# Kernel tuning notes

Hardware: AMD Instinct MI355X
Metric: run time of the kernel (lower is better)

The kernel has to match this reference:

```python
import jax, jax.numpy as jnp
import numpy as np

B, T, H, C = 2048, 1024, 512, 9
ZD, SD, GD = 128, 128, 16
COND = ZD + SD + GD  # hidden_fc input dim


def _gru_cell(x, h, w_ih, w_hh, b_ih, b_hh):
    # torch.nn.GRUCell math
    gi = x @ w_ih.T + b_ih          # [B, 3H]
    gh = h @ w_hh.T + b_hh          # [B, 3H]
    i_r, i_z, i_n = jnp.split(gi, 3, axis=-1)
    h_r, h_z, h_n = jnp.split(gh, 3, axis=-1)
    r = jax.nn.sigmoid(i_r + h_r)
    zg = jax.nn.sigmoid(i_z + h_z)
    n = jnp.tanh(i_n + r * h_n)
    return (1.0 - zg) * n + zg * h


def setup_inputs() -> dict:
    key = jax.random.key(0)
    ks = jax.random.split(key, 16)
    s = 0.05
    f32 = jnp.float32
    return {
        "z": jax.random.normal(ks[0], (B, ZD), f32),
        "skel_encoded": jax.random.normal(ks[1], (B, SD), f32),
        "skel": jax.random.uniform(ks[2], (B, T, C), f32),
        "cond": jax.random.normal(ks[3], (B, GD), f32),
        "rand_seq": jax.random.uniform(ks[4], (T, B, C), f32),
        "W_h": jax.random.normal(ks[5], (H, COND), f32) * s,
        "b_h": jnp.zeros((H,), f32),
        "w_ih1": jax.random.normal(ks[6], (3 * H, 2 * C), f32) * s,
        "w_hh1": jax.random.normal(ks[7], (3 * H, H), f32) * s,
        "b_ih1": jnp.zeros((3 * H,), f32),
        "b_hh1": jnp.zeros((3 * H,), f32),
        "w_ih2": jax.random.normal(ks[8], (3 * H, H), f32) * s,
        "w_hh2": jax.random.normal(ks[9], (3 * H, H), f32) * s,
        "b_ih2": jnp.zeros((3 * H,), f32),
        "b_hh2": jnp.zeros((3 * H,), f32),
        "W_out": jax.random.normal(ks[10], (C, H), f32) * s,
        "b_out": jnp.zeros((C,), f32),
    }


def reference(z, skel_encoded, skel, cond, rand_seq, W_h, b_h,
              w_ih1, w_hh1, b_ih1, b_hh1, w_ih2, w_hh2, b_ih2, b_hh2,
              W_out, b_out):
    b = z.shape[0]
    zc = jnp.concatenate([z.reshape(b, -1), skel_encoded, cond], axis=-1)
    h1_0 = jnp.tanh(zc @ W_h.T + b_h)                 # init hidden for gru1
    h2_0 = jnp.zeros_like(h1_0)                       # replaced at step 0
    out0 = jnp.zeros((b, C), z.dtype)
    skel_t = jnp.transpose(skel, (1, 0, 2))           # [T, B, C]

    def step(carry, xs):
        h1, h2, out = carry
        sk, rnd, i = xs
        x = jnp.concatenate([out, sk], axis=-1)       # [B, 2C]
        h1 = _gru_cell(x, h1, w_ih1, w_hh1, b_ih1, b_hh1)
        h2 = jnp.where(i == 0, h1, h2)                # hx[1] = hx[0] at i==0
        h2 = _gru_cell(h1, h2, w_ih2, w_hh2, b_ih2, b_hh2)
        note = jnp.tanh(h2) @ W_out.T + b_out         # out_fc (dropout=0 in eval)
        out = (jax.nn.sigmoid(note) - rnd > 0).astype(note.dtype)  # Bernoulli sample
        return (h1, h2, out), note

    _, notes = jax.lax.scan(step, (h1_0, h2_0, out0),
                            (skel_t, rand_seq, jnp.arange(T)))
    return jnp.transpose(notes, (1, 0, 2))            # [B, T, C]
```

## Files before the change

### kernel.cpp

```cpp
#include <hip/hip_runtime.h>
#include <math.h>

#define B_TOT 2048
#define T_LEN 1024
#define HID   512
#define CH    9
#define CONDK 272
#define K1X   (2*CH)
#define G3    1536
#define ROWS  8
#define NWG   (B_TOT/ROWS)
#define NTHR  512

#define SZ_W1T  ((HID + K1X) * G3)
#define SZ_W2T  ((2*HID) * G3)
#define SZ_WHT  (CONDK * HID)
#define OFF_W1T 0
#define OFF_W2T (OFF_W1T + SZ_W1T)
#define OFF_WHT (OFF_W2T + SZ_W2T)

__global__ void prep_kernel(const float* __restrict__ w_ih1, const float* __restrict__ w_hh1,
                            const float* __restrict__ w_ih2, const float* __restrict__ w_hh2,
                            const float* __restrict__ W_h, float* __restrict__ ws)
{
    int i = blockIdx.x * blockDim.x + threadIdx.x;
    const int total = SZ_W1T + SZ_W2T + SZ_WHT;
    if (i >= total) return;
    if (i < SZ_W1T) {
        int k = i / G3, g = i % G3;
        ws[OFF_W1T + i] = (k < HID) ? w_hh1[g*HID + k] : w_ih1[g*K1X + (k - HID)];
    } else if (i < SZ_W1T + SZ_W2T) {
        int j = i - SZ_W1T;
        int k = j / G3, g = j % G3;
        ws[OFF_W2T + j] = (k < HID) ? w_hh2[g*HID + k] : w_ih2[g*HID + (k - HID)];
    } else {
        int j = i - SZ_W1T - SZ_W2T;
        int k = j / HID, u = j % HID;
        ws[OFF_WHT + j] = W_h[u*CONDK + k];
    }
}

__device__ __forceinline__ float sigmf(float x) { return 1.0f / (1.0f + expf(-x)); }

__global__ __launch_bounds__(NTHR, 2)
void note_decoder_kernel(const float* __restrict__ z, const float* __restrict__ se,
                         const float* __restrict__ skel, const float* __restrict__ cond,
                         const float* __restrict__ rnd,
                         const float* __restrict__ b_h,
                         const float* __restrict__ b_ih1, const float* __restrict__ b_hh1,
                         const float* __restrict__ b_ih2, const float* __restrict__ b_hh2,
                         const float* __restrict__ W_out, const float* __restrict__ b_out,
                         const float* __restrict__ ws,
                         float* __restrict__ out)
{
    __shared__ float h1s[HID][ROWS];
    __shared__ float h2s[HID][ROWS];
    __shared__ float xf[2*CH][ROWS];
    __shared__ float wouts[HID][CH];

    const float* __restrict__ W1t = ws + OFF_W1T;
    const float* __restrict__ W2t = ws + OFF_W2T;
    const float* __restrict__ Wht = ws + OFF_WHT;

    const int tid  = threadIdx.x;
    const int row0 = blockIdx.x * ROWS;

    for (int i = tid; i < CH*HID; i += NTHR) {
        int c = i / HID, u = i % HID;
        wouts[u][c] = W_out[i];
    }
    for (int i = tid; i < ROWS*CONDK; i += NTHR) {
        int b = i / CONDK, k = i % CONDK;
        float v;
        if (k < 128)       v = z[(row0 + b)*128 + k];
        else if (k < 256)  v = se[(row0 + b)*128 + (k - 128)];
        else               v = cond[(row0 + b)*16 + (k - 256)];
        h2s[k][b] = v;
    }
    if (tid < ROWS*CH) xf[tid % CH][tid / CH] = 0.0f;
    __syncthreads();

    {
        float acc[ROWS];
        #pragma unroll
        for (int b = 0; b < ROWS; ++b) acc[b] = 0.0f;
        for (int k = 0; k < CONDK; ++k) {
            float w = Wht[k*HID + tid];
            float4 a0 = *(const float4*)&h2s[k][0];
            float4 a1 = *(const float4*)&h2s[k][4];
            float hv[ROWS] = {a0.x,a0.y,a0.z,a0.w,a1.x,a1.y,a1.z,a1.w};
            #pragma unroll
            for (int b = 0; b < ROWS; ++b) acc[b] = fmaf(hv[b], w, acc[b]);
        }
        float bh = b_h[tid];
        __syncthreads();
        #pragma unroll
        for (int b = 0; b < ROWS; ++b) acc[b] = tanhf(acc[b] + bh);
        *(float4*)&h1s[tid][0] = make_float4(acc[0],acc[1],acc[2],acc[3]);
        *(float4*)&h1s[tid][4] = make_float4(acc[4],acc[5],acc[6],acc[7]);
    }
    __syncthreads();

    const float br1 = b_ih1[tid]         + b_hh1[tid];
    const float bz1 = b_ih1[HID + tid]   + b_hh1[HID + tid];
    const float bi1 = b_ih1[2*HID + tid];
    const float bn1 = b_hh1[2*HID + tid];
    const float br2 = b_ih2[tid]         + b_hh2[tid];
    const float bz2 = b_ih2[HID + tid]   + b_hh2[HID + tid];
    const float bi2 = b_ih2[2*HID + tid];
    const float bn2 = b_hh2[2*HID + tid];

    const int wv = tid >> 6, ln = tid & 63;

    for (int t = 0; t < T_LEN; ++t) {
        if (tid < ROWS*CH) {
            int b = tid / CH, c = tid % CH;
            xf[CH + c][b] = skel[((size_t)(row0 + b)*T_LEN + t)*CH + c];
        }
        __syncthreads();

        float ar[ROWS], az[ROWS], ai[ROWS], ah[ROWS];
        #pragma unroll
        for (int b = 0; b < ROWS; ++b) { ar[b]=0.f; az[b]=0.f; ai[b]=0.f; ah[b]=0.f; }
        #pragma unroll 4
        for (int k = 0; k < HID; ++k) {
            const float* wr = W1t + (size_t)k*G3;
            float w_r = wr[tid], w_z = wr[HID + tid], w_n = wr[2*HID + tid];
            float4 a0 = *(const float4*)&h1s[k][0];
            float4 a1 = *(const float4*)&h1s[k][4];
            float hv[ROWS] = {a0.x,a0.y,a0.z,a0.w,a1.x,a1.y,a1.z,a1.w};
            #pragma unroll
            for (int b = 0; b < ROWS; ++b) {
                ar[b] = fmaf(hv[b], w_r, ar[b]);
                az[b] = fmaf(hv[b], w_z, az[b]);
                ah[b] = fmaf(hv[b], w_n, ah[b]);
            }
        }
        #pragma unroll
        for (int k = 0; k < K1X; ++k) {
            const float* wr = W1t + (size_t)(HID + k)*G3;
            float w_r = wr[tid], w_z = wr[HID + tid], w_n = wr[2*HID + tid];
            float4 a0 = *(const float4*)&xf[k][0];
            float4 a1 = *(const float4*)&xf[k][4];
            float xv[ROWS] = {a0.x,a0.y,a0.z,a0.w,a1.x,a1.y,a1.z,a1.w};
            #pragma unroll
            for (int b = 0; b < ROWS; ++b) {
                ar[b] = fmaf(xv[b], w_r, ar[b]);
                az[b] = fmaf(xv[b], w_z, az[b]);
                ai[b] = fmaf(xv[b], w_n, ai[b]);
            }
        }
        float4 p0 = *(const float4*)&h1s[tid][0];
        float4 p1 = *(const float4*)&h1s[tid][4];
        float h1old[ROWS] = {p0.x,p0.y,p0.z,p0.w,p1.x,p1.y,p1.z,p1.w};
        float h1n[ROWS];
        #pragma unroll
        for (int b = 0; b < ROWS; ++b) {
            float r  = sigmf(ar[b] + br1);
            float zg = sigmf(az[b] + bz1);
            float n  = tanhf(fmaf(r, ah[b] + bn1, ai[b] + bi1));
            h1n[b] = (1.0f - zg)*n + zg*h1old[b];
        }
        __syncthreads();
        *(float4*)&h1s[tid][0] = make_float4(h1n[0],h1n[1],h1n[2],h1n[3]);
        *(float4*)&h1s[tid][4] = make_float4(h1n[4],h1n[5],h1n[6],h1n[7]);
        if (t == 0) {
            *(float4*)&h2s[tid][0] = make_float4(h1n[0],h1n[1],h1n[2],h1n[3]);
            *(float4*)&h2s[tid][4] = make_float4(h1n[4],h1n[5],h1n[6],h1n[7]);
        }
        __syncthreads();

        #pragma unroll
        for (int b = 0; b < ROWS; ++b) { ar[b]=0.f; az[b]=0.f; ai[b]=0.f; ah[b]=0.f; }
        #pragma unroll 4
        for (int k = 0; k < HID; ++k) {
            const float* wr = W2t + (size_t)k*G3;
            float w_r = wr[tid], w_z = wr[HID + tid], w_n = wr[2*HID + tid];
            float4 a0 = *(const float4*)&h2s[k][0];
            float4 a1 = *(const float4*)&h2s[k][4];
            float hv[ROWS] = {a0.x,a0.y,a0.z,a0.w,a1.x,a1.y,a1.z,a1.w};
            #pragma unroll
            for (int b = 0; b < ROWS; ++b) {
                ar[b] = fmaf(hv[b], w_r, ar[b]);
                az[b] = fmaf(hv[b], w_z, az[b]);
                ah[b] = fmaf(hv[b], w_n, ah[b]);
            }
        }
        #pragma unroll 4
        for (int k = 0; k < HID; ++k) {
            const float* wr = W2t + (size_t)(HID + k)*G3;
            float w_r = wr[tid], w_z = wr[HID + tid], w_n = wr[2*HID + tid];
            float4 a0 = *(const float4*)&h1s[k][0];
            float4 a1 = *(const float4*)&h1s[k][4];
            float hv[ROWS] = {a0.x,a0.y,a0.z,a0.w,a1.x,a1.y,a1.z,a1.w};
            #pragma unroll
            for (int b = 0; b < ROWS; ++b) {
                ar[b] = fmaf(hv[b], w_r, ar[b]);
                az[b] = fmaf(hv[b], w_z, az[b]);
                ai[b] = fmaf(hv[b], w_n, ai[b]);
            }
        }
        float4 q0 = *(const float4*)&h2s[tid][0];
        float4 q1 = *(const float4*)&h2s[tid][4];
        float h2old[ROWS] = {q0.x,q0.y,q0.z,q0.w,q1.x,q1.y,q1.z,q1.w};
        float h2n[ROWS];
        #pragma unroll
        for (int b = 0; b < ROWS; ++b) {
            float r  = sigmf(ar[b] + br2);
            float zg = sigmf(az[b] + bz2);
            float n  = tanhf(fmaf(r, ah[b] + bn2, ai[b] + bi2));
            h2n[b] = (1.0f - zg)*n + zg*h2old[b];
        }
        __syncthreads();
        *(float4*)&h2s[tid][0] = make_float4(h2n[0],h2n[1],h2n[2],h2n[3]);
        *(float4*)&h2s[tid][4] = make_float4(h2n[4],h2n[5],h2n[6],h2n[7]);
        __syncthreads();

        {
            float na[CH];
            #pragma unroll
            for (int c = 0; c < CH; ++c) na[c] = 0.0f;
            for (int kk = ln; kk < HID; kk += 64) {
                float th = tanhf(h2s[kk][wv]);
                #pragma unroll
                for (int c = 0; c < CH; ++c) na[c] = fmaf(th, wouts[kk][c], na[c]);
            }
            #pragma unroll
            for (int c = 0; c < CH; ++c) {
                #pragma unroll
                for (int off = 32; off; off >>= 1)
                    na[c] += __shfl_xor(na[c], off, 64);
            }
            if (ln < CH) {
                int c = ln;
                float note = na[c] + b_out[c];
                float sg = sigmf(note);
                float rv = rnd[((size_t)t*B_TOT + row0 + wv)*CH + c];
                xf[c][wv] = (sg - rv > 0.0f) ? 1.0f : 0.0f;
                out[((size_t)(row0 + wv)*T_LEN + t)*CH + c] = note;
            }
        }
        __syncthreads();
    }
}

extern "C" void kernel_launch(void* const* d_in, const int* in_sizes, int n_in,
                              void* d_out, int out_size, void* d_ws, size_t ws_size,
                              hipStream_t stream)
{
    const float* z     = (const float*)d_in[0];
    const float* se    = (const float*)d_in[1];
    const float* skel  = (const float*)d_in[2];
    const float* cond  = (const float*)d_in[3];
    const float* rnd   = (const float*)d_in[4];
    const float* W_h   = (const float*)d_in[5];
    const float* b_h   = (const float*)d_in[6];
    const float* w_ih1 = (const float*)d_in[7];
    const float* w_hh1 = (const float*)d_in[8];
    const float* b_ih1 = (const float*)d_in[9];
    const float* b_hh1 = (const float*)d_in[10];
    const float* w_ih2 = (const float*)d_in[11];
    const float* w_hh2 = (const float*)d_in[12];
    const float* b_ih2 = (const float*)d_in[13];
    const float* b_hh2 = (const float*)d_in[14];
    const float* W_out = (const float*)d_in[15];
    const float* b_out = (const float*)d_in[16];
    float* ws  = (float*)d_ws;
    float* out = (float*)d_out;

    const int total = SZ_W1T + SZ_W2T + SZ_WHT;
    prep_kernel<<<(total + 255)/256, 256, 0, stream>>>(w_ih1, w_hh1, w_ih2, w_hh2, W_h, ws);
    note_decoder_kernel<<<NWG, NTHR, 0, stream>>>(z, se, skel, cond, rnd, b_h,
                                                  b_ih1, b_hh1, b_ih2, b_hh2,
                                                  W_out, b_out, ws, out);
}
```

Measured before the change: 192.4 ms.

## Split batch rows across thread pairs and interleave gate weights per unit

```diff
diff --git a/kernel.cpp b/kernel.cpp
--- a/kernel.cpp
+++ b/kernel.cpp
@@ -6,43 +6,47 @@
 #define HID   512
 #define CH    9
 #define CONDK 272
-#define K1X   (2*CH)
-#define G3    1536
 #define ROWS  8
 #define NWG   (B_TOT/ROWS)
-#define NTHR  512
-
-#define SZ_W1T  ((HID + K1X) * G3)
-#define SZ_W2T  ((2*HID) * G3)
+#define NTHR  1024
+
+#define K1TOT (HID + 18)
+#define K2TOT (2*HID)
+#define SZ_W1P  (K1TOT * HID * 3)
+#define SZ_W2P  (K2TOT * HID * 3)
 #define SZ_WHT  (CONDK * HID)
-#define OFF_W1T 0
-#define OFF_W2T (OFF_W1T + SZ_W1T)
-#define OFF_WHT (OFF_W2T + SZ_W2T)
+#define OFF_W1P 0
+#define OFF_W2P (OFF_W1P + SZ_W1P)
+#define OFF_WHT (OFF_W2P + SZ_W2P)
 
 __global__ void prep_kernel(const float* __restrict__ w_ih1, const float* __restrict__ w_hh1,
                             const float* __restrict__ w_ih2, const float* __restrict__ w_hh2,
                             const float* __restrict__ W_h, float* __restrict__ ws)
 {
     int i = blockIdx.x * blockDim.x + threadIdx.x;
-    const int total = SZ_W1T + SZ_W2T + SZ_WHT;
+    const int total = SZ_W1P + SZ_W2P + SZ_WHT;
     if (i >= total) return;
-    if (i < SZ_W1T) {
-        int k = i / G3, g = i % G3;
-        ws[OFF_W1T + i] = (k < HID) ? w_hh1[g*HID + k] : w_ih1[g*K1X + (k - HID)];
-    } else if (i < SZ_W1T + SZ_W2T) {
-        int j = i - SZ_W1T;
-        int k = j / G3, g = j % G3;
-        ws[OFF_W2T + j] = (k < HID) ? w_hh2[g*HID + k] : w_ih2[g*HID + (k - HID)];
+    if (i < SZ_W1P) {
+        int g = i % 3, rest = i / 3;
+        int u = rest % HID, k = rest / HID;
+        ws[OFF_W1P + i] = (k < HID) ? w_hh1[(size_t)(g*HID + u)*HID + k]
+                                    : w_ih1[(size_t)(g*HID + u)*18  + (k - HID)];
+    } else if (i < SZ_W1P + SZ_W2P) {
+        int j = i - SZ_W1P;
+        int g = j % 3, rest = j / 3;
+        int u = rest % HID, k = rest / HID;
+        ws[OFF_W2P + j] = (k < HID) ? w_hh2[(size_t)(g*HID + u)*HID + k]
+                                    : w_ih2[(size_t)(g*HID + u)*HID + (k - HID)];
     } else {
-        int j = i - SZ_W1T - SZ_W2T;
+        int j = i - SZ_W1P - SZ_W2P;
         int k = j / HID, u = j % HID;
-        ws[OFF_WHT + j] = W_h[u*CONDK + k];
+        ws[OFF_WHT + j] = W_h[(size_t)u*CONDK + k];
     }
 }
 
 __device__ __forceinline__ float sigmf(float x) { return 1.0f / (1.0f + expf(-x)); }
 
-__global__ __launch_bounds__(NTHR, 2)
+__global__ __launch_bounds__(NTHR, 4)
 void note_decoder_kernel(const float* __restrict__ z, const float* __restrict__ se,
                          const float* __restrict__ skel, const float* __restrict__ cond,
                          const float* __restrict__ rnd,
@@ -53,21 +57,23 @@
                          const float* __restrict__ ws,
                          float* __restrict__ out)
 {
-    __shared__ float h1s[HID][ROWS];
-    __shared__ float h2s[HID][ROWS];
+    __shared__ float hs[2][HID][ROWS];
     __shared__ float xf[2*CH][ROWS];
     __shared__ float wouts[HID][CH];
 
-    const float* __restrict__ W1t = ws + OFF_W1T;
-    const float* __restrict__ W2t = ws + OFF_W2T;
+    const float* __restrict__ W1p = ws + OFF_W1P;
+    const float* __restrict__ W2p = ws + OFF_W2P;
     const float* __restrict__ Wht = ws + OFF_WHT;
 
     const int tid  = threadIdx.x;
+    const int half = tid & 1;
+    const int u    = tid >> 1;
+    const int b0   = half * 4;
     const int row0 = blockIdx.x * ROWS;
 
     for (int i = tid; i < CH*HID; i += NTHR) {
-        int c = i / HID, u = i % HID;
-        wouts[u][c] = W_out[i];
+        int c = i / HID, uu = i % HID;
+        wouts[uu][c] = W_out[i];
     }
     for (int i = tid; i < ROWS*CONDK; i += NTHR) {
         int b = i / CONDK, k = i % CONDK;
@@ -75,40 +81,37 @@
         if (k < 128)       v = z[(row0 + b)*128 + k];
         else if (k < 256)  v = se[(row0 + b)*128 + (k - 128)];
         else               v = cond[(row0 + b)*16 + (k - 256)];
-        h2s[k][b] = v;
+        hs[1][k][b] = v;
     }
     if (tid < ROWS*CH) xf[tid % CH][tid / CH] = 0.0f;
     __syncthreads();
 
     {
-        float acc[ROWS];
-        #pragma unroll
-        for (int b = 0; b < ROWS; ++b) acc[b] = 0.0f;
+        float acc[4] = {0.f, 0.f, 0.f, 0.f};
+        #pragma unroll 4
         for (int k = 0; k < CONDK; ++k) {
-            float w = Wht[k*HID + tid];
-            float4 a0 = *(const float4*)&h2s[k][0];
-            float4 a1 = *(const float4*)&h2s[k][4];
-            float hv[ROWS] = {a0.x,a0.y,a0.z,a0.w,a1.x,a1.y,a1.z,a1.w};
-            #pragma unroll
-            for (int b = 0; b < ROWS; ++b) acc[b] = fmaf(hv[b], w, acc[b]);
-        }
-        float bh = b_h[tid];
-        __syncthreads();
-        #pragma unroll
-        for (int b = 0; b < ROWS; ++b) acc[b] = tanhf(acc[b] + bh);
-        *(float4*)&h1s[tid][0] = make_float4(acc[0],acc[1],acc[2],acc[3]);
-        *(float4*)&h1s[tid][4] = make_float4(acc[4],acc[5],acc[6],acc[7]);
-    }
-    __syncthreads();
-
-    const float br1 = b_ih1[tid]         + b_hh1[tid];
-    const float bz1 = b_ih1[HID + tid]   + b_hh1[HID + tid];
-    const float bi1 = b_ih1[2*HID + tid];
-    const float bn1 = b_hh1[2*HID + tid];
-    const float br2 = b_ih2[tid]         + b_hh2[tid];
-    const float bz2 = b_ih2[HID + tid]   + b_hh2[HID + tid];
-    const float bi2 = b_ih2[2*HID + tid];
-    const float bn2 = b_hh2[2*HID + tid];
+            float w = Wht[k*HID + u];
+            float4 a = *(const float4*)&hs[1][k][b0];
+            acc[0] = fmaf(a.x, w, acc[0]);
+            acc[1] = fmaf(a.y, w, acc[1]);
+            acc[2] = fmaf(a.z, w, acc[2]);
+            acc[3] = fmaf(a.w, w, acc[3]);
+        }
+        float bh = b_h[u];
+        __syncthreads();
+        #pragma unroll
+        for (int j = 0; j < 4; ++j) acc[j] = tanhf(acc[j] + bh);
+        *(float4*)&hs[0][u][b0] = make_float4(acc[0], acc[1], acc[2], acc[3]);
+    }
+
+    const float br1 = b_ih1[u]         + b_hh1[u];
+    const float bz1 = b_ih1[HID + u]   + b_hh1[HID + u];
+    const float bi1 = b_ih1[2*HID + u];
+    const float bn1 = b_hh1[2*HID + u];
+    const float br2 = b_ih2[u]         + b_hh2[u];
+    const float bz2 = b_ih2[HID + u]   + b_hh2[HID + u];
+    const float bi2 = b_ih2[2*HID + u];
+    const float bn2 = b_hh2[2*HID + u];
 
     const int wv = tid >> 6, ln = tid & 63;
 
@@ -119,109 +122,83 @@
         }
         __syncthreads();
 
-        float ar[ROWS], az[ROWS], ai[ROWS], ah[ROWS];
-        #pragma unroll
-        for (int b = 0; b < ROWS; ++b) { ar[b]=0.f; az[b]=0.f; ai[b]=0.f; ah[b]=0.f; }
+        float ar[4], az[4], ai[4], ah[4];
+        #pragma unroll
+        for (int j = 0; j < 4; ++j) { ar[j]=0.f; az[j]=0.f; ai[j]=0.f; ah[j]=0.f; }
         #pragma unroll 4
         for (int k = 0; k < HID; ++k) {
-            const float* wr = W1t + (size_t)k*G3;
-            float w_r = wr[tid], w_z = wr[HID + tid], w_n = wr[2*HID + tid];
-            float4 a0 = *(const float4*)&h1s[k][0];
-            float4 a1 = *(const float4*)&h1s[k][4];
-            float hv[ROWS] = {a0.x,a0.y,a0.z,a0.w,a1.x,a1.y,a1.z,a1.w};
-            #pragma unroll
-            for (int b = 0; b < ROWS; ++b) {
-                ar[b] = fmaf(hv[b], w_r, ar[b]);
-                az[b] = fmaf(hv[b], w_z, az[b]);
-                ah[b] = fmaf(hv[b], w_n, ah[b]);
-            }
-        }
-        #pragma unroll
-        for (int k = 0; k < K1X; ++k) {
-            const float* wr = W1t + (size_t)(HID + k)*G3;
-            float w_r = wr[tid], w_z = wr[HID + tid], w_n = wr[2*HID + tid];
-            float4 a0 = *(const float4*)&xf[k][0];
-            float4 a1 = *(const float4*)&xf[k][4];
-            float xv[ROWS] = {a0.x,a0.y,a0.z,a0.w,a1.x,a1.y,a1.z,a1.w};
-            #pragma unroll
-            for (int b = 0; b < ROWS; ++b) {
-                ar[b] = fmaf(xv[b], w_r, ar[b]);
-                az[b] = fmaf(xv[b], w_z, az[b]);
-                ai[b] = fmaf(xv[b], w_n, ai[b]);
-            }
-        }
-        float4 p0 = *(const float4*)&h1s[tid][0];
-        float4 p1 = *(const float4*)&h1s[tid][4];
-        float h1old[ROWS] = {p0.x,p0.y,p0.z,p0.w,p1.x,p1.y,p1.z,p1.w};
-        float h1n[ROWS];
-        #pragma unroll
-        for (int b = 0; b < ROWS; ++b) {
-            float r  = sigmf(ar[b] + br1);
-            float zg = sigmf(az[b] + bz1);
-            float n  = tanhf(fmaf(r, ah[b] + bn1, ai[b] + bi1));
-            h1n[b] = (1.0f - zg)*n + zg*h1old[b];
-        }
-        __syncthreads();
-        *(float4*)&h1s[tid][0] = make_float4(h1n[0],h1n[1],h1n[2],h1n[3]);
-        *(float4*)&h1s[tid][4] = make_float4(h1n[4],h1n[5],h1n[6],h1n[7]);
-        if (t == 0) {
-            *(float4*)&h2s[tid][0] = make_float4(h1n[0],h1n[1],h1n[2],h1n[3]);
-            *(float4*)&h2s[tid][4] = make_float4(h1n[4],h1n[5],h1n[6],h1n[7]);
-        }
-        __syncthreads();
-
-        #pragma unroll
-        for (int b = 0; b < ROWS; ++b) { ar[b]=0.f; az[b]=0.f; ai[b]=0.f; ah[b]=0.f; }
+            float3 w = *(const float3*)(W1p + ((size_t)k*HID + u)*3);
+            float4 a = *(const float4*)&hs[0][k][b0];
+            ar[0]=fmaf(a.x,w.x,ar[0]); az[0]=fmaf(a.x,w.y,az[0]); ah[0]=fmaf(a.x,w.z,ah[0]);
+            ar[1]=fmaf(a.y,w.x,ar[1]); az[1]=fmaf(a.y,w.y,az[1]); ah[1]=fmaf(a.y,w.z,ah[1]);
+            ar[2]=fmaf(a.z,w.x,ar[2]); az[2]=fmaf(a.z,w.y,az[2]); ah[2]=fmaf(a.z,w.z,ah[2]);
+            ar[3]=fmaf(a.w,w.x,ar[3]); az[3]=fmaf(a.w,w.y,az[3]); ah[3]=fmaf(a.w,w.z,ah[3]);
+        }
+        #pragma unroll
+        for (int i = 0; i < 18; ++i) {
+            float3 w = *(const float3*)(W1p + ((size_t)(HID + i)*HID + u)*3);
+            float4 a = *(const float4*)&xf[i][b0];
+            ar[0]=fmaf(a.x,w.x,ar[0]); az[0]=fmaf(a.x,w.y,az[0]); ai[0]=fmaf(a.x,w.z,ai[0]);
+            ar[1]=fmaf(a.y,w.x,ar[1]); az[1]=fmaf(a.y,w.y,az[1]); ai[1]=fmaf(a.y,w.z,ai[1]);
+            ar[2]=fmaf(a.z,w.x,ar[2]); az[2]=fmaf(a.z,w.y,az[2]); ai[2]=fmaf(a.z,w.z,ai[2]);
+            ar[3]=fmaf(a.w,w.x,ar[3]); az[3]=fmaf(a.w,w.y,az[3]); ai[3]=fmaf(a.w,w.z,ai[3]);
+        }
+        float4 p = *(const float4*)&hs[0][u][b0];
+        float h1old[4] = {p.x, p.y, p.z, p.w};
+        float h1n[4];
+        #pragma unroll
+        for (int j = 0; j < 4; ++j) {
+            float r  = sigmf(ar[j] + br1);
+            float zg = sigmf(az[j] + bz1);
+            float n  = tanhf(fmaf(r, ah[j] + bn1, ai[j] + bi1));
+            h1n[j] = (1.0f - zg)*n + zg*h1old[j];
+        }
+        __syncthreads();
+        *(float4*)&hs[0][u][b0] = make_float4(h1n[0], h1n[1], h1n[2], h1n[3]);
+        if (t == 0)
+            *(float4*)&hs[1][u][b0] = make_float4(h1n[0], h1n[1], h1n[2], h1n[3]);
+        __syncthreads();
+
+        #pragma unroll
+        for (int j = 0; j < 4; ++j) { ar[j]=0.f; az[j]=0.f; ai[j]=0.f; ah[j]=0.f; }
         #pragma unroll 4
         for (int k = 0; k < HID; ++k) {
-            const float* wr = W2t + (size_t)k*G3;
-            float w_r = wr[tid], w_z = wr[HID + tid], w_n = wr[2*HID + tid];
-            float4 a0 = *(const float4*)&h2s[k][0];
-            float4 a1 = *(const float4*)&h2s[k][4];
-            float hv[ROWS] = {a0.x,a0.y,a0.z,a0.w,a1.x,a1.y,a1.z,a1.w};
-            #pragma unroll
-            for (int b = 0; b < ROWS; ++b) {
-                ar[b] = fmaf(hv[b], w_r, ar[b]);
-                az[b] = fmaf(hv[b], w_z, az[b]);
-                ah[b] = fmaf(hv[b], w_n, ah[b]);
-            }
+            float3 w = *(const float3*)(W2p + ((size_t)k*HID + u)*3);
+            float4 a = *(const float4*)&hs[1][k][b0];
+            ar[0]=fmaf(a.x,w.x,ar[0]); az[0]=fmaf(a.x,w.y,az[0]); ah[0]=fmaf(a.x,w.z,ah[0]);
+            ar[1]=fmaf(a.y,w.x,ar[1]); az[1]=fmaf(a.y,w.y,az[1]); ah[1]=fmaf(a.y,w.z,ah[1]);
+            ar[2]=fmaf(a.z,w.x,ar[2]); az[2]=fmaf(a.z,w.y,az[2]); ah[2]=fmaf(a.z,w.z,ah[2]);
+            ar[3]=fmaf(a.w,w.x,ar[3]); az[3]=fmaf(a.w,w.y,az[3]); ah[3]=fmaf(a.w,w.z,ah[3]);
         }
         #pragma unroll 4
         for (int k = 0; k < HID; ++k) {
-            const float* wr = W2t + (size_t)(HID + k)*G3;
-            float w_r = wr[tid], w_z = wr[HID + tid], w_n = wr[2*HID + tid];
-            float4 a0 = *(const float4*)&h1s[k][0];
-            float4 a1 = *(const float4*)&h1s[k][4];
-            float hv[ROWS] = {a0.x,a0.y,a0.z,a0.w,a1.x,a1.y,a1.z,a1.w};
-            #pragma unroll
-            for (int b = 0; b < ROWS; ++b) {
-                ar[b] = fmaf(hv[b], w_r, ar[b]);
-                az[b] = fmaf(hv[b], w_z, az[b]);
-                ai[b] = fmaf(hv[b], w_n, ai[b]);
-            }
-        }
-        float4 q0 = *(const float4*)&h2s[tid][0];
-        float4 q1 = *(const float4*)&h2s[tid][4];
-        float h2old[ROWS] = {q0.x,q0.y,q0.z,q0.w,q1.x,q1.y,q1.z,q1.w};
-        float h2n[ROWS];
-        #pragma unroll
-        for (int b = 0; b < ROWS; ++b) {
-            float r  = sigmf(ar[b] + br2);
-            float zg = sigmf(az[b] + bz2);
-            float n  = tanhf(fmaf(r, ah[b] + bn2, ai[b] + bi2));
-            h2n[b] = (1.0f - zg)*n + zg*h2old[b];
-        }
-        __syncthreads();
-        *(float4*)&h2s[tid][0] = make_float4(h2n[0],h2n[1],h2n[2],h2n[3]);
-        *(float4*)&h2s[tid][4] = make_float4(h2n[4],h2n[5],h2n[6],h2n[7]);
-        __syncthreads();
-
-        {
+            float3 w = *(const float3*)(W2p + ((size_t)(HID + k)*HID + u)*3);
+            float4 a = *(const float4*)&hs[0][k][b0];
+            ar[0]=fmaf(a.x,w.x,ar[0]); az[0]=fmaf(a.x,w.y,az[0]); ai[0]=fmaf(a.x,w.z,ai[0]);
+            ar[1]=fmaf(a.y,w.x,ar[1]); az[1]=fmaf(a.y,w.y,az[1]); ai[1]=fmaf(a.y,w.z,ai[1]);
+            ar[2]=fmaf(a.z,w.x,ar[2]); az[2]=fmaf(a.z,w.y,az[2]); ai[2]=fmaf(a.z,w.z,ai[2]);
+            ar[3]=fmaf(a.w,w.x,ar[3]); az[3]=fmaf(a.w,w.y,az[3]); ai[3]=fmaf(a.w,w.z,ai[3]);
+        }
+        float4 q = *(const float4*)&hs[1][u][b0];
+        float h2old[4] = {q.x, q.y, q.z, q.w};
+        float h2n[4];
+        #pragma unroll
+        for (int j = 0; j < 4; ++j) {
+            float r  = sigmf(ar[j] + br2);
+            float zg = sigmf(az[j] + bz2);
+            float n  = tanhf(fmaf(r, ah[j] + bn2, ai[j] + bi2));
+            h2n[j] = (1.0f - zg)*n + zg*h2old[j];
+        }
+        __syncthreads();
+        *(float4*)&hs[1][u][b0] = make_float4(h2n[0], h2n[1], h2n[2], h2n[3]);
+        __syncthreads();
+
+        if (tid < 512) {
             float na[CH];
             #pragma unroll
             for (int c = 0; c < CH; ++c) na[c] = 0.0f;
             for (int kk = ln; kk < HID; kk += 64) {
-                float th = tanhf(h2s[kk][wv]);
+                float th = tanhf(hs[1][kk][wv]);
                 #pragma unroll
                 for (int c = 0; c < CH; ++c) na[c] = fmaf(th, wouts[kk][c], na[c]);
             }
@@ -268,7 +245,7 @@
     float* ws  = (float*)d_ws;
     float* out = (float*)d_out;
 
-    const int total = SZ_W1T + SZ_W2T + SZ_WHT;
+    const int total = SZ_W1P + SZ_W2P + SZ_WHT;
     prep_kernel<<<(total + 255)/256, 256, 0, stream>>>(w_ih1, w_hh1, w_ih2, w_hh2, W_h, ws);
     note_decoder_kernel<<<NWG, NTHR, 0, stream>>>(z, se, skel, cond, rnd, b_h,
                                                   b_ih1, b_hh1, b_ih2, b_hh2,
```

Result: slower. 500.7 ms (+160.2%).

## Double-buffer GRU weight tiles into LDS via async global_load_lds prefetch

Applied to the files above, without the earlier changes.

```diff
diff --git a/kernel.cpp b/kernel.cpp
--- a/kernel.cpp
+++ b/kernel.cpp
@@ -11,6 +11,9 @@
 #define ROWS  8
 #define NWG   (B_TOT/ROWS)
 #define NTHR  512
+#define PF    8
+#define NT1   (HID/PF)
+#define NT2   (2*HID/PF)
 
 #define SZ_W1T  ((HID + K1X) * G3)
 #define SZ_W2T  ((2*HID) * G3)
@@ -42,6 +45,45 @@
 
 __device__ __forceinline__ float sigmf(float x) { return 1.0f / (1.0f + expf(-x)); }
 
+typedef __attribute__((address_space(1))) const unsigned int g_u32;
+typedef __attribute__((address_space(3))) unsigned int l_u32;
+__device__ __forceinline__ void gload_lds16(const void* g, void* l) {
+    __builtin_amdgcn_global_load_lds((g_u32*)g, (l_u32*)l, 16, 0, 0);
+}
+
+#define WAIT6 asm volatile("s_waitcnt vmcnt(6)" ::: "memory")
+#define WAIT0 asm volatile("s_waitcnt vmcnt(0)" ::: "memory")
+
+#define ISSUE(PANEL, K0, BUF)                                                     \
+    {                                                                             \
+        const float* pb_ = (PANEL) + (size_t)(K0)*G3;                             \
+        _Pragma("unroll")                                                         \
+        for (int r_ = 0; r_ < 6; ++r_)                                            \
+            gload_lds16(pb_ + choff[r_], &Wb[BUF][w][r_*256]);                    \
+    }
+
+#define CTILE(HS, A2, K0, BUF)                                                    \
+    {                                                                             \
+        const float* Wsl_ = &Wb[BUF][w][0];                                       \
+        _Pragma("unroll")                                                         \
+        for (int j_ = 0; j_ < PF; ++j_) {                                         \
+            float w_r = Wsl_[(j_*3+0)*64 + ln];                                   \
+            float w_z = Wsl_[(j_*3+1)*64 + ln];                                   \
+            float w_n = Wsl_[(j_*3+2)*64 + ln];                                   \
+            int k_ = (K0) + j_;                                                   \
+            float4 a0 = *(const float4*)&HS[k_][0];                               \
+            float4 a1 = *(const float4*)&HS[k_][4];                               \
+            ar[0]=fmaf(a0.x,w_r,ar[0]); az[0]=fmaf(a0.x,w_z,az[0]); A2[0]=fmaf(a0.x,w_n,A2[0]); \
+            ar[1]=fmaf(a0.y,w_r,ar[1]); az[1]=fmaf(a0.y,w_z,az[1]); A2[1]=fmaf(a0.y,w_n,A2[1]); \
+            ar[2]=fmaf(a0.z,w_r,ar[2]); az[2]=fmaf(a0.z,w_z,az[2]); A2[2]=fmaf(a0.z,w_n,A2[2]); \
+            ar[3]=fmaf(a0.w,w_r,ar[3]); az[3]=fmaf(a0.w,w_z,az[3]); A2[3]=fmaf(a0.w,w_n,A2[3]); \
+            ar[4]=fmaf(a1.x,w_r,ar[4]); az[4]=fmaf(a1.x,w_z,az[4]); A2[4]=fmaf(a1.x,w_n,A2[4]); \
+            ar[5]=fmaf(a1.y,w_r,ar[5]); az[5]=fmaf(a1.y,w_z,az[5]); A2[5]=fmaf(a1.y,w_n,A2[5]); \
+            ar[6]=fmaf(a1.z,w_r,ar[6]); az[6]=fmaf(a1.z,w_z,az[6]); A2[6]=fmaf(a1.z,w_n,A2[6]); \
+            ar[7]=fmaf(a1.w,w_r,ar[7]); az[7]=fmaf(a1.w,w_z,az[7]); A2[7]=fmaf(a1.w,w_n,A2[7]); \
+        }                                                                         \
+    }
+
 __global__ __launch_bounds__(NTHR, 2)
 void note_decoder_kernel(const float* __restrict__ z, const float* __restrict__ se,
                          const float* __restrict__ skel, const float* __restrict__ cond,
@@ -53,6 +95,7 @@
                          const float* __restrict__ ws,
                          float* __restrict__ out)
 {
+    __shared__ float Wb[2][8][PF*3*64];
     __shared__ float h1s[HID][ROWS];
     __shared__ float h2s[HID][ROWS];
     __shared__ float xf[2*CH][ROWS];
@@ -63,7 +106,17 @@
     const float* __restrict__ Wht = ws + OFF_WHT;
 
     const int tid  = threadIdx.x;
+    const int w    = tid >> 6;
+    const int ln   = tid & 63;
     const int row0 = blockIdx.x * ROWS;
+
+    int choff[6];
+    #pragma unroll
+    for (int r = 0; r < 6; ++r) {
+        int c = 4*r + (ln >> 4);
+        int j = c / 3, s = c - 3*j;
+        choff[r] = j*G3 + s*HID + w*64 + (ln & 15)*4;
+    }
 
     for (int i = tid; i < CH*HID; i += NTHR) {
         int c = i / HID, u = i % HID;
@@ -85,12 +138,12 @@
         #pragma unroll
         for (int b = 0; b < ROWS; ++b) acc[b] = 0.0f;
         for (int k = 0; k < CONDK; ++k) {
-            float w = Wht[k*HID + tid];
+            float wv_ = Wht[k*HID + tid];
             float4 a0 = *(const float4*)&h2s[k][0];
             float4 a1 = *(const float4*)&h2s[k][4];
             float hv[ROWS] = {a0.x,a0.y,a0.z,a0.w,a1.x,a1.y,a1.z,a1.w};
             #pragma unroll
-            for (int b = 0; b < ROWS; ++b) acc[b] = fmaf(hv[b], w, acc[b]);
+            for (int b = 0; b < ROWS; ++b) acc[b] = fmaf(hv[b], wv_, acc[b]);
         }
         float bh = b_h[tid];
         __syncthreads();
@@ -110,8 +163,6 @@
     const float bi2 = b_ih2[2*HID + tid];
     const float bn2 = b_hh2[2*HID + tid];
 
-    const int wv = tid >> 6, ln = tid & 63;
-
     for (int t = 0; t < T_LEN; ++t) {
         if (tid < ROWS*CH) {
             int b = tid / CH, c = tid % CH;
@@ -122,33 +173,29 @@
         float ar[ROWS], az[ROWS], ai[ROWS], ah[ROWS];
         #pragma unroll
         for (int b = 0; b < ROWS; ++b) { ar[b]=0.f; az[b]=0.f; ai[b]=0.f; ah[b]=0.f; }
-        #pragma unroll 4
-        for (int k = 0; k < HID; ++k) {
-            const float* wr = W1t + (size_t)k*G3;
-            float w_r = wr[tid], w_z = wr[HID + tid], w_n = wr[2*HID + tid];
-            float4 a0 = *(const float4*)&h1s[k][0];
-            float4 a1 = *(const float4*)&h1s[k][4];
-            float hv[ROWS] = {a0.x,a0.y,a0.z,a0.w,a1.x,a1.y,a1.z,a1.w};
-            #pragma unroll
-            for (int b = 0; b < ROWS; ++b) {
-                ar[b] = fmaf(hv[b], w_r, ar[b]);
-                az[b] = fmaf(hv[b], w_z, az[b]);
-                ah[b] = fmaf(hv[b], w_n, ah[b]);
-            }
-        }
+        ISSUE(W1t, 0, 0);
+        ISSUE(W1t, PF, 1);
+        for (int i = 0; i < NT1 - 2; ++i) {
+            WAIT6;
+            CTILE(h1s, ah, i*PF, (i & 1));
+            ISSUE(W1t, (i+2)*PF, (i & 1));
+        }
+        WAIT6; CTILE(h1s, ah, (NT1-2)*PF, 0);
+        WAIT0; CTILE(h1s, ah, (NT1-1)*PF, 1);
         #pragma unroll
         for (int k = 0; k < K1X; ++k) {
             const float* wr = W1t + (size_t)(HID + k)*G3;
             float w_r = wr[tid], w_z = wr[HID + tid], w_n = wr[2*HID + tid];
-            float4 a0 = *(const float4*)&xf[k][0];
+            float4 a  = *(const float4*)&xf[k][0];
             float4 a1 = *(const float4*)&xf[k][4];
-            float xv[ROWS] = {a0.x,a0.y,a0.z,a0.w,a1.x,a1.y,a1.z,a1.w};
-            #pragma unroll
-            for (int b = 0; b < ROWS; ++b) {
-                ar[b] = fmaf(xv[b], w_r, ar[b]);
-                az[b] = fmaf(xv[b], w_z, az[b]);
-                ai[b] = fmaf(xv[b], w_n, ai[b]);
-            }
+            ar[0]=fmaf(a.x,w_r,ar[0]);  az[0]=fmaf(a.x,w_z,az[0]);  ai[0]=fmaf(a.x,w_n,ai[0]);
+            ar[1]=fmaf(a.y,w_r,ar[1]);  az[1]=fmaf(a.y,w_z,az[1]);  ai[1]=fmaf(a.y,w_n,ai[1]);
+            ar[2]=fmaf(a.z,w_r,ar[2]);  az[2]=fmaf(a.z,w_z,az[2]);  ai[2]=fmaf(a.z,w_n,ai[2]);
+            ar[3]=fmaf(a.w,w_r,ar[3]);  az[3]=fmaf(a.w,w_z,az[3]);  ai[3]=fmaf(a.w,w_n,ai[3]);
+            ar[4]=fmaf(a1.x,w_r,ar[4]); az[4]=fmaf(a1.x,w_z,az[4]); ai[4]=fmaf(a1.x,w_n,ai[4]);
+            ar[5]=fmaf(a1.y,w_r,ar[5]); az[5]=fmaf(a1.y,w_z,az[5]); ai[5]=fmaf(a1.y,w_n,ai[5]);
+            ar[6]=fmaf(a1.z,w_r,ar[6]); az[6]=fmaf(a1.z,w_z,az[6]); ai[6]=fmaf(a1.z,w_n,ai[6]);
+            ar[7]=fmaf(a1.w,w_r,ar[7]); az[7]=fmaf(a1.w,w_z,az[7]); ai[7]=fmaf(a1.w,w_n,ai[7]);
         }
         float4 p0 = *(const float4*)&h1s[tid][0];
         float4 p1 = *(const float4*)&h1s[tid][4];
@@ -172,34 +219,20 @@
 
         #pragma unroll
         for (int b = 0; b < ROWS; ++b) { ar[b]=0.f; az[b]=0.f; ai[b]=0.f; ah[b]=0.f; }
-        #pragma unroll 4
-        for (int k = 0; k < HID; ++k) {
-            const float* wr = W2t + (size_t)k*G3;
-            float w_r = wr[tid], w_z = wr[HID + tid], w_n = wr[2*HID + tid];
-            float4 a0 = *(const float4*)&h2s[k][0];
-            float4 a1 = *(const float4*)&h2s[k][4];
-            float hv[ROWS] = {a0.x,a0.y,a0.z,a0.w,a1.x,a1.y,a1.z,a1.w};
-            #pragma unroll
-            for (int b = 0; b < ROWS; ++b) {
-                ar[b] = fmaf(hv[b], w_r, ar[b]);
-                az[b] = fmaf(hv[b], w_z, az[b]);
-                ah[b] = fmaf(hv[b], w_n, ah[b]);
-            }
-        }
-        #pragma unroll 4
-        for (int k = 0; k < HID; ++k) {
-            const float* wr = W2t + (size_t)(HID + k)*G3;
-            float w_r = wr[tid], w_z = wr[HID + tid], w_n = wr[2*HID + tid];
-            float4 a0 = *(const float4*)&h1s[k][0];
-            float4 a1 = *(const float4*)&h1s[k][4];
-            float hv[ROWS] = {a0.x,a0.y,a0.z,a0.w,a1.x,a1.y,a1.z,a1.w};
-            #pragma unroll
-            for (int b = 0; b < ROWS; ++b) {
-                ar[b] = fmaf(hv[b], w_r, ar[b]);
-                az[b] = fmaf(hv[b], w_z, az[b]);
-                ai[b] = fmaf(hv[b], w_n, ai[b]);
-            }
-        }
+        ISSUE(W2t, 0, 0);
+        ISSUE(W2t, PF, 1);
+        for (int i = 0; i < NT2/2; ++i) {
+            WAIT6;
+            CTILE(h2s, ah, i*PF, (i & 1));
+            ISSUE(W2t, (i+2)*PF, (i & 1));
+        }
+        for (int i = NT2/2; i < NT2 - 2; ++i) {
+            WAIT6;
+            CTILE(h1s, ai, (i - NT2/2)*PF, (i & 1));
+            ISSUE(W2t, (i+2)*PF, (i & 1));
+        }
+        WAIT6; CTILE(h1s, ai, (NT2/2 - 2)*PF, 0);
+        WAIT0; CTILE(h1s, ai, (NT2/2 - 1)*PF, 1);
         float4 q0 = *(const float4*)&h2s[tid][0];
         float4 q1 = *(const float4*)&h2s[tid][4];
         float h2old[ROWS] = {q0.x,q0.y,q0.z,q0.w,q1.x,q1.y,q1.z,q1.w};
@@ -221,7 +254,7 @@
             #pragma unroll
             for (int c = 0; c < CH; ++c) na[c] = 0.0f;
             for (int kk = ln; kk < HID; kk += 64) {
-                float th = tanhf(h2s[kk][wv]);
+                float th = tanhf(h2s[kk][w]);
                 #pragma unroll
                 for (int c = 0; c < CH; ++c) na[c] = fmaf(th, wouts[kk][c], na[c]);
             }
@@ -235,9 +268,9 @@
                 int c = ln;
                 float note = na[c] + b_out[c];
                 float sg = sigmf(note);
-                float rv = rnd[((size_t)t*B_TOT + row0 + wv)*CH + c];
-                xf[c][wv] = (sg - rv > 0.0f) ? 1.0f : 0.0f;
-                out[((size_t)(row0 + wv)*T_LEN + t)*CH + c] = note;
+                float rv = rnd[((size_t)t*B_TOT + row0 + w)*CH + c];
+                xf[c][w] = (sg - rv > 0.0f) ? 1.0f : 0.0f;
+                out[((size_t)(row0 + w)*T_LEN + t)*CH + c] = note;
             }
         }
         __syncthreads();
```

After: 285.6 ms. 48.4% more time.
